# Optimization experiments

Measured on AMD Instinct MI355X. Metric: run time of the kernel, lower is better.

The kernel has to match this reference:

```python
import jax, jax.numpy as jnp
import numpy as np


def setup_inputs() -> dict:
    key = jax.random.key(0)
    ks = jax.random.split(key, 6)
    B, H, W, C = 4, 64, 64, 256
    D = 256 // 4  # inter_channel // 4
    return {
        "g": jax.random.normal(ks[0], (B, H, W, C), dtype=jnp.float32),
        "x": jax.random.normal(ks[1], (B, H, W, C), dtype=jnp.float32),
        "x_query": jax.random.normal(ks[2], (B, H, W, D), dtype=jnp.float32),
        "phi_g": jax.random.normal(ks[3], (B, H, W, D), dtype=jnp.float32),
        "x_value": jax.random.normal(ks[4], (B, H, W, C), dtype=jnp.float32),
        "k": jax.random.normal(ks[5], (1,), dtype=jnp.float32),
    }


def reference(g, x, x_query, phi_g, x_value, k):
    B, H, W, C = x.shape
    D = x_query.shape[-1]
    HW = H * W
    q = x_query.reshape(B, HW, D)
    pg = phi_g.reshape(B, HW, D)
    v = x_value.reshape(B, HW, C)
    # scale[b,i,j] = sum_d phi_g[b,i,d] * x_query[b,j,d]  -> (B, HW, HW)
    scale = jnp.einsum("bid,bjd->bij", pg, q)
    soft = jax.nn.softmax(scale, axis=-1)
    # scaled_value[b,i,c] = sum_j soft[b,i,j] * v[b,j,c]
    sv = jnp.einsum("bij,bjc->bic", soft, v).reshape(B, H, W, C)
    layero = k * sv + x
    return jnp.concatenate([layero, g], axis=3)
```

## Files before the change

### kernel.cpp

```cpp
#include <hip/hip_runtime.h>

#define N_  4096
#define D_  64
#define C_  256

typedef short bf16x8 __attribute__((ext_vector_type(8)));
typedef float f32x4  __attribute__((ext_vector_type(4)));

__device__ __forceinline__ unsigned short f2bf(float f) {
    union { float f; unsigned int i; } v; v.f = f;
    unsigned int r = v.i + 0x7fffu + ((v.i >> 16) & 1u);
    return (unsigned short)(r >> 16);
}

__global__ void prepass_kernel(const float* __restrict__ xq,
                               const float* __restrict__ pg,
                               const float* __restrict__ xv,
                               unsigned short* __restrict__ qbf,
                               unsigned short* __restrict__ pgbf,
                               unsigned short* __restrict__ vt2) {
    __shared__ float s[128][65];
    const int bid = blockIdx.x;
    const int t   = threadIdx.x;
    if (bid < 512) {
        const float* src = (bid < 256) ? xq : pg;
        unsigned short* dst = (bid < 256) ? qbf : pgbf;
        const int base = (bid & 255) * 1024 + t;
#pragma unroll
        for (int it = 0; it < 4; ++it) {
            const int i = base + it * 256;
            float4 v = ((const float4*)src)[i];
            ushort4 o;
            o.x = f2bf(v.x); o.y = f2bf(v.y); o.z = f2bf(v.z); o.w = f2bf(v.w);
            ((ushort4*)dst)[i] = o;
        }
        return;
    }
    const int tb = bid - 512;
    const int b  = tb >> 7;
    const int jt = (tb >> 2) & 31;
    const int cq = tb & 3;
    const int j0 = jt * 128, c0 = cq * 64;
#pragma unroll
    for (int it = 0; it < 8; ++it) {
        const int idx = it * 256 + t;
        const int jl  = idx >> 4;
        const int cl4 = (idx & 15) * 4;
        *(float4*)&s[jl][cl4] =
            *(const float4*)(xv + ((size_t)b * N_ + j0 + jl) * C_ + c0 + cl4);
    }
    __syncthreads();
    unsigned short* outb = vt2 + ((((size_t)b * 32 + jt) * 16 + cq * 4) * 4) * 512;
#pragma unroll
    for (int it = 0; it < 8; ++it) {
        const int ci   = it * 256 + t;
        const int frag = ci >> 7;
        const int rem  = ci & 127;
        const int L    = rem >> 1;
        const int eh   = (rem & 1) * 4;
        const int cbl  = frag >> 2, ks = frag & 3;
        const int cl   = cbl * 16 + (L & 15);
        const int jl   = ks * 32 + (L >> 4) * 8 + eh;
        ushort4 o;
        o.x = f2bf(s[jl + 0][cl]); o.y = f2bf(s[jl + 1][cl]);
        o.z = f2bf(s[jl + 2][cl]); o.w = f2bf(s[jl + 3][cl]);
        ((ushort4*)outb)[ci] = o;
    }
}

__global__ __launch_bounds__(512, 4) void attn_main(
    const float* __restrict__ g,  const float* __restrict__ x,
    const float* __restrict__ kk, float* __restrict__ out,
    const unsigned short* __restrict__ qbf,
    const unsigned short* __restrict__ pgbf,
    const unsigned short* __restrict__ vt2)
{
    __shared__ unsigned short p_lds[2][32][132];
    __shared__ float s_red[32][260];
    __shared__ float s_l[32];

    const int t    = threadIdx.x;
    const int lane = t & 63;
    const int w    = t >> 6;
    const int l15  = lane & 15;
    const int quad = lane >> 4;

    const int bid = blockIdx.x;
    const int b   = bid & 3;
    const int rg  = bid >> 2;
    const int i0  = rg * 32;
    const size_t rowbase = (size_t)b * N_ + i0;

    const int wsj = w;
    const int ctq = w & 3;
    const int ksh = w >> 2;

    if (t < 32) s_l[t] = 0.f;

#pragma unroll
    for (int it = 0; it < 4; ++it) {
        const int row = it * 8 + w;
        const int c4  = lane * 4;
        const float4 gv = *(const float4*)(g + (rowbase + row) * C_ + c4);
        *(float4*)(out + (rowbase + row) * (2 * C_) + C_ + c4) = gv;
    }

    bf16x8 pgf[2][2];
#pragma unroll
    for (int mt = 0; mt < 2; ++mt)
#pragma unroll
        for (int ks = 0; ks < 2; ++ks)
            pgf[mt][ks] = *(const bf16x8*)(pgbf +
                (rowbase + mt * 16 + l15) * D_ + ks * 32 + quad * 8);

    f32x4 oacc[2][4];
#pragma unroll
    for (int mt = 0; mt < 2; ++mt)
#pragma unroll
        for (int ct = 0; ct < 4; ++ct) oacc[mt][ct] = (f32x4){0.f, 0.f, 0.f, 0.f};
    float ls[2][4] = {{0.f,0.f,0.f,0.f},{0.f,0.f,0.f,0.f}};

    const unsigned short* qb  = qbf + (size_t)b * N_ * D_;
    const unsigned short* vtb = vt2 + (size_t)b * N_ * C_;

    __syncthreads();

    for (int jt = 0; jt < 32; ++jt) {
        const int j0  = jt * 128;
        const int buf = jt & 1;
        const unsigned short* tbase = vtb + (size_t)jt * 32768;

        bf16x8 vfp[2][4];
#pragma unroll
        for (int kp = 0; kp < 2; ++kp)
#pragma unroll
            for (int c2 = 0; c2 < 4; ++c2)
                vfp[kp][c2] = *(const bf16x8*)(tbase +
                    (size_t)(((ctq * 4 + c2) * 4) + (ksh * 2 + kp)) * 512 + lane * 8);

        f32x4 sacc[2];
        sacc[0] = (f32x4){0.f,0.f,0.f,0.f};
        sacc[1] = (f32x4){0.f,0.f,0.f,0.f};
#pragma unroll
        for (int ks = 0; ks < 2; ++ks) {
            const bf16x8 qf = *(const bf16x8*)(qb +
                (size_t)(j0 + wsj * 16 + l15) * D_ + ks * 32 + quad * 8);
            sacc[0] = __builtin_amdgcn_mfma_f32_16x16x32_bf16(pgf[0][ks], qf, sacc[0], 0, 0, 0);
            sacc[1] = __builtin_amdgcn_mfma_f32_16x16x32_bf16(pgf[1][ks], qf, sacc[1], 0, 0, 0);
        }
#pragma unroll
        for (int mt = 0; mt < 2; ++mt)
#pragma unroll
            for (int r = 0; r < 4; ++r) {
                const float p = __expf(sacc[mt][r]);
                ls[mt][r] += p;
                p_lds[buf][mt * 16 + quad * 4 + r][wsj * 16 + l15] = f2bf(p);
            }
        __syncthreads();

#pragma unroll
        for (int kp = 0; kp < 2; ++kp) {
            const int kk2 = (ksh * 2 + kp) * 32;
            union { bf16x8 f; uint2 u2[2]; } pa[2];
#pragma unroll
            for (int mt = 0; mt < 2; ++mt) {
                const unsigned short* prow = &p_lds[buf][mt * 16 + l15][kk2 + quad * 8];
                pa[mt].u2[0] = *(const uint2*)prow;
                pa[mt].u2[1] = *(const uint2*)(prow + 4);
            }
#pragma unroll
            for (int c2 = 0; c2 < 4; ++c2) {
                oacc[0][c2] = __builtin_amdgcn_mfma_f32_16x16x32_bf16(pa[0].f, vfp[kp][c2], oacc[0][c2], 0, 0, 0);
                oacc[1][c2] = __builtin_amdgcn_mfma_f32_16x16x32_bf16(pa[1].f, vfp[kp][c2], oacc[1][c2], 0, 0, 0);
            }
        }
    }

#pragma unroll
    for (int mt = 0; mt < 2; ++mt)
#pragma unroll
        for (int r = 0; r < 4; ++r) {
            float s = ls[mt][r];
            s += __shfl_xor(s, 1); s += __shfl_xor(s, 2);
            s += __shfl_xor(s, 4); s += __shfl_xor(s, 8);
            if (l15 == 0) atomicAdd(&s_l[mt * 16 + quad * 4 + r], s);
        }

    if (ksh == 1) {
#pragma unroll
        for (int mt = 0; mt < 2; ++mt)
#pragma unroll
            for (int ct = 0; ct < 4; ++ct)
#pragma unroll
                for (int r = 0; r < 4; ++r)
                    s_red[mt * 16 + quad * 4 + r][ctq * 64 + ct * 16 + l15] = oacc[mt][ct][r];
    }
    __syncthreads();

    if (ksh == 0) {
        const float kval = kk[0];
#pragma unroll
        for (int mt = 0; mt < 2; ++mt)
#pragma unroll
            for (int r = 0; r < 4; ++r) {
                const int m = mt * 16 + quad * 4 + r;
                const float linv = 1.f / s_l[m];
                const size_t row = rowbase + m;
#pragma unroll
                for (int ct = 0; ct < 4; ++ct) {
                    const int c = ctq * 64 + ct * 16 + l15;
                    const float o = oacc[mt][ct][r] + s_red[m][c];
                    out[row * (2 * C_) + c] = kval * (o * linv) + x[row * C_ + c];
                }
            }
    }
}

#define ROWS 4
#define FNT  256
__global__ __launch_bounds__(FNT, 2) void attn_fallback(
    const float* __restrict__ g, const float* __restrict__ x,
    const float* __restrict__ xq, const float* __restrict__ pg,
    const float* __restrict__ xv, const float* __restrict__ kk,
    float* __restrict__ out)
{
    __shared__ __align__(16) float s_pg[ROWS][D_];
    __shared__ __align__(16) float s_sc[N_ * ROWS];
    __shared__ float s_rmax[4][ROWS];
    __shared__ float s_rsum[4][ROWS];

    const int t = threadIdx.x, lane = t & 63, w = t >> 6, blk = blockIdx.x;
    const int b = blk >> 10, i0 = (blk & 1023) * ROWS;
    const size_t rowbase = (size_t)b * N_ + i0;
    {
        const int r = t >> 6, cc = (t & 63) * 4;
        const float4 gv = *(const float4*)(g + (rowbase + r) * C_ + cc);
        *(float4*)(out + (rowbase + r) * (2 * C_) + C_ + cc) = gv;
    }
    { const int r = t >> 6, d = t & 63; s_pg[r][d] = pg[(rowbase + r) * D_ + d]; }
    __syncthreads();
    const float* qb = xq + (size_t)b * N_ * D_;
    float lmax[ROWS];
#pragma unroll
    for (int r = 0; r < ROWS; ++r) lmax[r] = -1e30f;
    for (int jj = 0; jj < N_ / FNT; ++jj) {
        const int j = t + jj * FNT;
        const float4* q4p = (const float4*)(qb + (size_t)j * D_);
        float s[ROWS] = {0.f, 0.f, 0.f, 0.f};
#pragma unroll
        for (int u = 0; u < D_ / 8; ++u) {
            const float4 qa = q4p[u * 2], qc = q4p[u * 2 + 1];
#pragma unroll
            for (int r = 0; r < ROWS; ++r) {
                const float4 pa = *(const float4*)&s_pg[r][u * 8];
                const float4 pb = *(const float4*)&s_pg[r][u * 8 + 4];
                s[r] += qa.x * pa.x + qa.y * pa.y + qa.z * pa.z + qa.w * pa.w
                      + qc.x * pb.x + qc.y * pb.y + qc.z * pb.z + qc.w * pb.w;
            }
        }
        *(float4*)&s_sc[j * ROWS] = make_float4(s[0], s[1], s[2], s[3]);
#pragma unroll
        for (int r = 0; r < ROWS; ++r) lmax[r] = fmaxf(lmax[r], s[r]);
    }
#pragma unroll
    for (int r = 0; r < ROWS; ++r) {
        float m = lmax[r];
        for (int o = 32; o > 0; o >>= 1) m = fmaxf(m, __shfl_down(m, o));
        if (lane == 0) s_rmax[w][r] = m;
    }
    __syncthreads();
    float bmax[ROWS];
#pragma unroll
    for (int r = 0; r < ROWS; ++r)
        bmax[r] = fmaxf(fmaxf(s_rmax[0][r], s_rmax[1][r]), fmaxf(s_rmax[2][r], s_rmax[3][r]));
    float lsum[ROWS] = {0.f, 0.f, 0.f, 0.f};
    for (int jj = 0; jj < N_ / FNT; ++jj) {
        const int j = t + jj * FNT;
        float4 s4 = *(const float4*)&s_sc[j * ROWS];
        s4.x = __expf(s4.x - bmax[0]); s4.y = __expf(s4.y - bmax[1]);
        s4.z = __expf(s4.z - bmax[2]); s4.w = __expf(s4.w - bmax[3]);
        *(float4*)&s_sc[j * ROWS] = s4;
        lsum[0] += s4.x; lsum[1] += s4.y; lsum[2] += s4.z; lsum[3] += s4.w;
    }
#pragma unroll
    for (int r = 0; r < ROWS; ++r) {
        float sm = lsum[r];
        for (int o = 32; o > 0; o >>= 1) sm += __shfl_down(sm, o);
        if (lane == 0) s_rsum[w][r] = sm;
    }
    __syncthreads();
    float rinv[ROWS];
#pragma unroll
    for (int r = 0; r < ROWS; ++r)
        rinv[r] = 1.f / (s_rsum[0][r] + s_rsum[1][r] + s_rsum[2][r] + s_rsum[3][r]);
    const int jg = lane >> 4;
    const int c0 = (w * 16 + (lane & 15)) * 4;
    const float* vb = xv + (size_t)b * N_ * C_;
    float acc[ROWS][4];
#pragma unroll
    for (int r = 0; r < ROWS; ++r)
#pragma unroll
        for (int q = 0; q < 4; ++q) acc[r][q] = 0.f;
#pragma unroll 4
    for (int jj = 0; jj < N_ / 4; ++jj) {
        const int j = jj * 4 + jg;
        const float4 p4 = *(const float4*)&s_sc[j * ROWS];
        const float4 v4 = *(const float4*)(vb + (size_t)j * C_ + c0);
        acc[0][0] += p4.x * v4.x; acc[0][1] += p4.x * v4.y; acc[0][2] += p4.x * v4.z; acc[0][3] += p4.x * v4.w;
        acc[1][0] += p4.y * v4.x; acc[1][1] += p4.y * v4.y; acc[1][2] += p4.y * v4.z; acc[1][3] += p4.y * v4.w;
        acc[2][0] += p4.z * v4.x; acc[2][1] += p4.z * v4.y; acc[2][2] += p4.z * v4.z; acc[2][3] += p4.z * v4.w;
        acc[3][0] += p4.w * v4.x; acc[3][1] += p4.w * v4.y; acc[3][2] += p4.w * v4.z; acc[3][3] += p4.w * v4.w;
    }
#pragma unroll
    for (int r = 0; r < ROWS; ++r)
#pragma unroll
        for (int q = 0; q < 4; ++q) {
            acc[r][q] += __shfl_xor(acc[r][q], 16);
            acc[r][q] += __shfl_xor(acc[r][q], 32);
        }
    const float kval = kk[0];
    if (lane < 16) {
        const int c = (w * 16 + lane) * 4;
#pragma unroll
        for (int r = 0; r < ROWS; ++r) {
            const float4 xv4 = *(const float4*)(x + (rowbase + r) * C_ + c);
            float4 ov;
            ov.x = kval * (acc[r][0] * rinv[r]) + xv4.x;
            ov.y = kval * (acc[r][1] * rinv[r]) + xv4.y;
            ov.z = kval * (acc[r][2] * rinv[r]) + xv4.z;
            ov.w = kval * (acc[r][3] * rinv[r]) + xv4.w;
            *(float4*)(out + (rowbase + r) * (2 * C_) + c) = ov;
        }
    }
}

extern "C" void kernel_launch(void* const* d_in, const int* in_sizes, int n_in,
                              void* d_out, int out_size, void* d_ws, size_t ws_size,
                              hipStream_t stream) {
    const float* g  = (const float*)d_in[0];
    const float* x  = (const float*)d_in[1];
    const float* xq = (const float*)d_in[2];
    const float* pg = (const float*)d_in[3];
    const float* xv = (const float*)d_in[4];
    const float* kk = (const float*)d_in[5];
    float* out = (float*)d_out;

    const int B = in_sizes[0] / (N_ * C_);
    const size_t qn = (size_t)B * N_ * D_;
    const size_t vn = (size_t)B * N_ * C_;
    const size_t need = (2 * qn + vn) * sizeof(unsigned short);

    if (ws_size < need) {
        attn_fallback<<<dim3(B * (N_ / ROWS)), FNT, 0, stream>>>(g, x, xq, pg, xv, kk, out);
        return;
    }

    unsigned short* qbf  = (unsigned short*)d_ws;
    unsigned short* pgbf = qbf + qn;
    unsigned short* vt2  = pgbf + qn;

    prepass_kernel<<<dim3(512 + B * 128), 256, 0, stream>>>(xq, pg, xv, qbf, pgbf, vt2);
    attn_main<<<dim3(B * (N_ / 32)), 512, 0, stream>>>(g, x, kk, out, qbf, pgbf, vt2);
}
```

Before: 175.4 us.

## Double query-row tile to 64, drop split-K reduction, simplify V transpose prepass

The main attention kernel now handles 64 query rows per block instead of 32. Each wave computes four row tiles of scores and accumulates over all four k-slices of the PV product for half the rows, so the cross-wave LDS reduction buffer and its extra barrier are gone. This halves how often each block reads the V and Q tiles per output row. The Q fragment for the next tile is prefetched after the barrier. The V transpose prepass now writes each MFMA fragment straight from strided global loads without an LDS staging tile. The cost is higher register pressure (launch bounds lowered to 2 blocks), fewer blocks, and uncoalesced strided reads in the prepass.

```diff
diff --git a/kernel.cpp b/kernel.cpp
--- a/kernel.cpp
+++ b/kernel.cpp
@@ -19,7 +19,6 @@
                                unsigned short* __restrict__ qbf,
                                unsigned short* __restrict__ pgbf,
                                unsigned short* __restrict__ vt2) {
-    __shared__ float s[128][65];
     const int bid = blockIdx.x;
     const int t   = threadIdx.x;
     if (bid < 512) {
@@ -36,48 +35,37 @@
         }
         return;
     }
-    const int tb = bid - 512;
-    const int b  = tb >> 7;
-    const int jt = (tb >> 2) & 31;
-    const int cq = tb & 3;
-    const int j0 = jt * 128, c0 = cq * 64;
-#pragma unroll
-    for (int it = 0; it < 8; ++it) {
-        const int idx = it * 256 + t;
-        const int jl  = idx >> 4;
-        const int cl4 = (idx & 15) * 4;
-        *(float4*)&s[jl][cl4] =
-            *(const float4*)(xv + ((size_t)b * N_ + j0 + jl) * C_ + c0 + cl4);
-    }
-    __syncthreads();
-    unsigned short* outb = vt2 + ((((size_t)b * 32 + jt) * 16 + cq * 4) * 4) * 512;
-#pragma unroll
-    for (int it = 0; it < 8; ++it) {
-        const int ci   = it * 256 + t;
-        const int frag = ci >> 7;
-        const int rem  = ci & 127;
-        const int L    = rem >> 1;
-        const int eh   = (rem & 1) * 4;
-        const int cbl  = frag >> 2, ks = frag & 3;
-        const int cl   = cbl * 16 + (L & 15);
-        const int jl   = ks * 32 + (L >> 4) * 8 + eh;
-        ushort4 o;
-        o.x = f2bf(s[jl + 0][cl]); o.y = f2bf(s[jl + 1][cl]);
-        o.z = f2bf(s[jl + 2][cl]); o.w = f2bf(s[jl + 3][cl]);
-        ((ushort4*)outb)[ci] = o;
-    }
-}
-
-__global__ __launch_bounds__(512, 4) void attn_main(
+    const int lane = t & 63;
+    const int w    = t >> 6;
+    const int l15  = lane & 15;
+    const int quad = lane >> 4;
+    const int f    = (bid - 512) * 4 + w;
+    const int b    = f >> 11;
+    const int jt   = (f >> 6) & 31;
+    const int cb   = (f >> 2) & 15;
+    const int ks   = f & 3;
+    const int c    = cb * 16 + l15;
+    const int jb   = jt * 128 + ks * 32 + quad * 8;
+    const float* src = xv + ((size_t)b * N_ + jb) * C_ + c;
+    float v0 = src[0 * C_], v1 = src[1 * C_], v2 = src[2 * C_], v3 = src[3 * C_];
+    float v4 = src[4 * C_], v5 = src[5 * C_], v6 = src[6 * C_], v7 = src[7 * C_];
+    uint4 o;
+    o.x = (unsigned)f2bf(v0) | ((unsigned)f2bf(v1) << 16);
+    o.y = (unsigned)f2bf(v2) | ((unsigned)f2bf(v3) << 16);
+    o.z = (unsigned)f2bf(v4) | ((unsigned)f2bf(v5) << 16);
+    o.w = (unsigned)f2bf(v6) | ((unsigned)f2bf(v7) << 16);
+    *(uint4*)(vt2 + (size_t)f * 512 + lane * 8) = o;
+}
+
+__global__ __launch_bounds__(512, 2) void attn_main(
     const float* __restrict__ g,  const float* __restrict__ x,
     const float* __restrict__ kk, float* __restrict__ out,
     const unsigned short* __restrict__ qbf,
     const unsigned short* __restrict__ pgbf,
     const unsigned short* __restrict__ vt2)
 {
-    __shared__ unsigned short p_lds[2][32][132];
-    __shared__ float s_red[32][260];
-    __shared__ float s_l[32];
+    __shared__ unsigned short p_lds[2][64][132];
+    __shared__ float s_l[64];
 
     const int t    = threadIdx.x;
     const int lane = t & 63;
@@ -88,26 +76,26 @@
     const int bid = blockIdx.x;
     const int b   = bid & 3;
     const int rg  = bid >> 2;
-    const int i0  = rg * 32;
+    const int i0  = rg * 64;
     const size_t rowbase = (size_t)b * N_ + i0;
 
     const int wsj = w;
+    const int mh  = w >> 2;
     const int ctq = w & 3;
-    const int ksh = w >> 2;
-
-    if (t < 32) s_l[t] = 0.f;
-
-#pragma unroll
-    for (int it = 0; it < 4; ++it) {
+
+    if (t < 64) s_l[t] = 0.f;
+
+#pragma unroll
+    for (int it = 0; it < 8; ++it) {
         const int row = it * 8 + w;
         const int c4  = lane * 4;
         const float4 gv = *(const float4*)(g + (rowbase + row) * C_ + c4);
         *(float4*)(out + (rowbase + row) * (2 * C_) + C_ + c4) = gv;
     }
 
-    bf16x8 pgf[2][2];
-#pragma unroll
-    for (int mt = 0; mt < 2; ++mt)
+    bf16x8 pgf[4][2];
+#pragma unroll
+    for (int mt = 0; mt < 4; ++mt)
 #pragma unroll
         for (int ks = 0; ks < 2; ++ks)
             pgf[mt][ks] = *(const bf16x8*)(pgbf +
@@ -115,41 +103,48 @@
 
     f32x4 oacc[2][4];
 #pragma unroll
-    for (int mt = 0; mt < 2; ++mt)
-#pragma unroll
-        for (int ct = 0; ct < 4; ++ct) oacc[mt][ct] = (f32x4){0.f, 0.f, 0.f, 0.f};
-    float ls[2][4] = {{0.f,0.f,0.f,0.f},{0.f,0.f,0.f,0.f}};
+    for (int mtl = 0; mtl < 2; ++mtl)
+#pragma unroll
+        for (int ct = 0; ct < 4; ++ct) oacc[mtl][ct] = (f32x4){0.f, 0.f, 0.f, 0.f};
+    float ls[4][4];
+#pragma unroll
+    for (int mt = 0; mt < 4; ++mt)
+#pragma unroll
+        for (int r = 0; r < 4; ++r) ls[mt][r] = 0.f;
 
     const unsigned short* qb  = qbf + (size_t)b * N_ * D_;
     const unsigned short* vtb = vt2 + (size_t)b * N_ * C_;
 
+    bf16x8 qf[2];
+#pragma unroll
+    for (int ks = 0; ks < 2; ++ks)
+        qf[ks] = *(const bf16x8*)(qb + (size_t)(wsj * 16 + l15) * D_ + ks * 32 + quad * 8);
+
     __syncthreads();
 
     for (int jt = 0; jt < 32; ++jt) {
-        const int j0  = jt * 128;
         const int buf = jt & 1;
         const unsigned short* tbase = vtb + (size_t)jt * 32768;
 
-        bf16x8 vfp[2][4];
-#pragma unroll
-        for (int kp = 0; kp < 2; ++kp)
-#pragma unroll
-            for (int c2 = 0; c2 < 4; ++c2)
-                vfp[kp][c2] = *(const bf16x8*)(tbase +
-                    (size_t)(((ctq * 4 + c2) * 4) + (ksh * 2 + kp)) * 512 + lane * 8);
-
-        f32x4 sacc[2];
-        sacc[0] = (f32x4){0.f,0.f,0.f,0.f};
-        sacc[1] = (f32x4){0.f,0.f,0.f,0.f};
-#pragma unroll
-        for (int ks = 0; ks < 2; ++ks) {
-            const bf16x8 qf = *(const bf16x8*)(qb +
-                (size_t)(j0 + wsj * 16 + l15) * D_ + ks * 32 + quad * 8);
-            sacc[0] = __builtin_amdgcn_mfma_f32_16x16x32_bf16(pgf[0][ks], qf, sacc[0], 0, 0, 0);
-            sacc[1] = __builtin_amdgcn_mfma_f32_16x16x32_bf16(pgf[1][ks], qf, sacc[1], 0, 0, 0);
-        }
-#pragma unroll
-        for (int mt = 0; mt < 2; ++mt)
+        bf16x8 vfp[4][4];
+#pragma unroll
+        for (int ks = 0; ks < 4; ++ks)
+#pragma unroll
+            for (int ct = 0; ct < 4; ++ct)
+                vfp[ks][ct] = *(const bf16x8*)(tbase +
+                    (size_t)(((ctq * 4 + ct) * 4) + ks) * 512 + lane * 8);
+
+        f32x4 sacc[4];
+#pragma unroll
+        for (int mt = 0; mt < 4; ++mt) sacc[mt] = (f32x4){0.f, 0.f, 0.f, 0.f};
+#pragma unroll
+        for (int ks = 0; ks < 2; ++ks)
+#pragma unroll
+            for (int mt = 0; mt < 4; ++mt)
+                sacc[mt] = __builtin_amdgcn_mfma_f32_16x16x32_bf16(pgf[mt][ks], qf[ks], sacc[mt], 0, 0, 0);
+
+#pragma unroll
+        for (int mt = 0; mt < 4; ++mt)
 #pragma unroll
             for (int r = 0; r < 4; ++r) {
                 const float p = __expf(sacc[mt][r]);
@@ -158,26 +153,34 @@
             }
         __syncthreads();
 
-#pragma unroll
-        for (int kp = 0; kp < 2; ++kp) {
-            const int kk2 = (ksh * 2 + kp) * 32;
+        if (jt < 31) {
+            const int jn = (jt + 1) * 128;
+#pragma unroll
+            for (int ks = 0; ks < 2; ++ks)
+                qf[ks] = *(const bf16x8*)(qb +
+                    (size_t)(jn + wsj * 16 + l15) * D_ + ks * 32 + quad * 8);
+        }
+
+#pragma unroll
+        for (int ks = 0; ks < 4; ++ks) {
             union { bf16x8 f; uint2 u2[2]; } pa[2];
 #pragma unroll
-            for (int mt = 0; mt < 2; ++mt) {
-                const unsigned short* prow = &p_lds[buf][mt * 16 + l15][kk2 + quad * 8];
-                pa[mt].u2[0] = *(const uint2*)prow;
-                pa[mt].u2[1] = *(const uint2*)(prow + 4);
-            }
-#pragma unroll
-            for (int c2 = 0; c2 < 4; ++c2) {
-                oacc[0][c2] = __builtin_amdgcn_mfma_f32_16x16x32_bf16(pa[0].f, vfp[kp][c2], oacc[0][c2], 0, 0, 0);
-                oacc[1][c2] = __builtin_amdgcn_mfma_f32_16x16x32_bf16(pa[1].f, vfp[kp][c2], oacc[1][c2], 0, 0, 0);
-            }
-        }
-    }
-
-#pragma unroll
-    for (int mt = 0; mt < 2; ++mt)
+            for (int mtl = 0; mtl < 2; ++mtl) {
+                const unsigned short* prow =
+                    &p_lds[buf][(mh * 2 + mtl) * 16 + l15][ks * 32 + quad * 8];
+                pa[mtl].u2[0] = *(const uint2*)prow;
+                pa[mtl].u2[1] = *(const uint2*)(prow + 4);
+            }
+#pragma unroll
+            for (int ct = 0; ct < 4; ++ct) {
+                oacc[0][ct] = __builtin_amdgcn_mfma_f32_16x16x32_bf16(pa[0].f, vfp[ks][ct], oacc[0][ct], 0, 0, 0);
+                oacc[1][ct] = __builtin_amdgcn_mfma_f32_16x16x32_bf16(pa[1].f, vfp[ks][ct], oacc[1][ct], 0, 0, 0);
+            }
+        }
+    }
+
+#pragma unroll
+    for (int mt = 0; mt < 4; ++mt)
 #pragma unroll
         for (int r = 0; r < 4; ++r) {
             float s = ls[mt][r];
@@ -185,34 +188,23 @@
             s += __shfl_xor(s, 4); s += __shfl_xor(s, 8);
             if (l15 == 0) atomicAdd(&s_l[mt * 16 + quad * 4 + r], s);
         }
-
-    if (ksh == 1) {
-#pragma unroll
-        for (int mt = 0; mt < 2; ++mt)
-#pragma unroll
-            for (int ct = 0; ct < 4; ++ct)
-#pragma unroll
-                for (int r = 0; r < 4; ++r)
-                    s_red[mt * 16 + quad * 4 + r][ctq * 64 + ct * 16 + l15] = oacc[mt][ct][r];
-    }
-    __syncthreads();
-
-    if (ksh == 0) {
-        const float kval = kk[0];
-#pragma unroll
-        for (int mt = 0; mt < 2; ++mt)
-#pragma unroll
-            for (int r = 0; r < 4; ++r) {
-                const int m = mt * 16 + quad * 4 + r;
-                const float linv = 1.f / s_l[m];
-                const size_t row = rowbase + m;
-#pragma unroll
-                for (int ct = 0; ct < 4; ++ct) {
-                    const int c = ctq * 64 + ct * 16 + l15;
-                    const float o = oacc[mt][ct][r] + s_red[m][c];
-                    out[row * (2 * C_) + c] = kval * (o * linv) + x[row * C_ + c];
-                }
-            }
+    __syncthreads();
+
+    const float kval = kk[0];
+#pragma unroll
+    for (int mtl = 0; mtl < 2; ++mtl) {
+        const int mt = mh * 2 + mtl;
+#pragma unroll
+        for (int r = 0; r < 4; ++r) {
+            const int m = mt * 16 + quad * 4 + r;
+            const float linv = 1.f / s_l[m];
+            const size_t row = rowbase + m;
+#pragma unroll
+            for (int ct = 0; ct < 4; ++ct) {
+                const int c = ctq * 64 + ct * 16 + l15;
+                out[row * (2 * C_) + c] = kval * (oacc[mtl][ct][r] * linv) + x[row * C_ + c];
+            }
+        }
     }
 }
 
@@ -359,6 +351,6 @@
     unsigned short* pgbf = qbf + qn;
     unsigned short* vt2  = pgbf + qn;
 
-    prepass_kernel<<<dim3(512 + B * 128), 256, 0, stream>>>(xq, pg, xv, qbf, pgbf, vt2);
-    attn_main<<<dim3(B * (N_ / 32)), 512, 0, stream>>>(g, x, kk, out, qbf, pgbf, vt2);
-}
+    prepass_kernel<<<dim3(512 + B * 512), 256, 0, stream>>>(xq, pg, xv, qbf, pgbf, vt2);
+    attn_main<<<dim3(B * (N_ / 64)), 512, 0, stream>>>(g, x, kk, out, qbf, pgbf, vt2);
+}
```

Result: no change. 173.3 us (-1.2%).
